# Optimization experiments

Measured on AMD Instinct MI355X. Metric: run time of the kernel, lower is better.

## Reference

```python
import jax, jax.numpy as jnp
import numpy as np

THRESHOLD = 0.95
B, T, H = 32, 2000, 512
NUM_TARGETS = 250.0  # alphas normalized so each row sums to this (mimics alpha *= num/_num)
MAX_LABEL_LEN = 256


def setup_inputs() -> dict:
    key = jax.random.key(0)
    k1, k2 = jax.random.split(key)
    hidden = jax.random.normal(k1, (B, T, H), dtype=jnp.float32)
    u = jax.random.uniform(k2, (B, T), dtype=jnp.float32)
    alphas = u / u.sum(-1, keepdims=True) * NUM_TARGETS  # per-row sum == NUM_TARGETS
    return {"hidden": hidden, "alphas": alphas, "max_label_len": MAX_LABEL_LEN}


def _cif(hidden, alphas, max_label_len, threshold=THRESHOLD):
    """Continuous integrate-and-fire: sequential scan over time + fire-gather."""
    Bn, Tn, Hn = hidden.shape

    def step(carry, inp):
        integrate, frame = carry              # [B], [B, H]
        alpha, h = inp                        # [B], [B, H]
        dist_completion = 1.0 - integrate
        integ = integrate + alpha
        fire = integ > threshold              # [B] bool
        cur = jnp.where(fire, dist_completion, alpha)
        remainds = alpha - cur
        frame_out = frame + cur[:, None] * h  # emitted frame at this step
        integ_next = jnp.where(fire, integ - 1.0, integ)
        frame_next = jnp.where(fire[:, None], remainds[:, None] * h, frame_out)
        return (integ_next, frame_next), (integ, frame_out)

    init = (jnp.zeros((Bn,), hidden.dtype), jnp.zeros((Bn, Hn), hidden.dtype))
    xs = (jnp.swapaxes(alphas, 0, 1), jnp.swapaxes(hidden, 0, 1))  # time-major
    _, (fires_t, frames_t) = jax.lax.scan(step, init, xs)
    fires = jnp.swapaxes(fires_t, 0, 1)    # [B, T]
    frames = jnp.swapaxes(frames_t, 0, 1)  # [B, T, H]

    # Gather fired frames per batch row, left-packed and zero-padded to max_label_len.
    mask = fires > threshold                               # [B, T]
    pos = jnp.cumsum(mask.astype(jnp.int32), axis=1) - 1   # running fire index
    pos = jnp.where(mask, pos, max_label_len)              # non-fires go to dump slot
    out = jnp.zeros((Bn, max_label_len + 1, Hn), hidden.dtype)
    out = out.at[jnp.arange(Bn)[:, None], pos].set(frames)
    return out[:, :max_label_len]  # drop dump slot -> [B, L, H]


def reference(hidden, alphas, max_label_len):
    return _cif(hidden, alphas, max_label_len)
```

## Files before the change

### kernel.cpp

```cpp
#include <hip/hip_runtime.h>
#include <stdint.h>

static constexpr int   Bn      = 32;
static constexpr int   Tn      = 2000;
static constexpr int   Hn      = 512;
static constexpr int   Ln      = 256;
static constexpr float kThresh = 0.95f;
static constexpr int   TCHUNK  = 40;
static constexpr int   NTCH    = Tn / TCHUNK;
static constexpr int   PCH     = 20;
static constexpr int   NPCH    = Tn / PCH;
static constexpr int   MSTRIDE = 64;
static constexpr unsigned PUBF = 0x40000000u;

__global__ __launch_bounds__(64, 1) void cif_fused_kernel(
    const float* __restrict__ hidden,
    const float* __restrict__ alphas,
    uint64_t* __restrict__ meta,
    float* __restrict__ out) {
  const int lane = threadIdx.x;
  __shared__ __align__(16) float alds[Tn];

  if (blockIdx.x < Bn) {
    __builtin_amdgcn_s_setprio(3);
    const int b = blockIdx.x;
    {
      const float4* __restrict__ arow =
          reinterpret_cast<const float4*>(alphas + (size_t)b * Tn);
      for (int i = lane; i < Tn / 4; i += 64)
        *reinterpret_cast<float4*>(&alds[4 * i]) = arow[i];
    }
    __syncthreads();

    float I  = 0.0f;
    int   fc = 0;
    float cur[PCH], nxt[PCH];
#pragma unroll
    for (int i = 0; i < PCH / 4; ++i) {
      const float4 v = *reinterpret_cast<const float4*>(&alds[4 * i]);
      cur[4 * i + 0] = v.x; cur[4 * i + 1] = v.y;
      cur[4 * i + 2] = v.z; cur[4 * i + 3] = v.w;
    }
    for (int c = 0; c < NPCH; ++c) {
      if (c + 1 < NPCH) {
#pragma unroll
        for (int i = 0; i < PCH / 4; ++i) {
          const float4 v = *reinterpret_cast<const float4*>(
              &alds[(c + 1) * PCH + 4 * i]);
          nxt[4 * i + 0] = v.x; nxt[4 * i + 1] = v.y;
          nxt[4 * i + 2] = v.z; nxt[4 * i + 3] = v.w;
        }
      }
      if ((c & 1) == 0 && lane == 0) {
        const uint64_t v = ((uint64_t)__float_as_uint(I) << 32) |
                           (uint64_t)(PUBF | (unsigned)fc);
        __hip_atomic_store(&meta[(size_t)b * MSTRIDE + (c >> 1)], v,
                           __ATOMIC_RELAXED, __HIP_MEMORY_SCOPE_AGENT);
      }
#pragma unroll
      for (int j = 0; j < PCH; ++j) {
        const float integ = I + cur[j];
        const bool  fire  = integ > kThresh;
        I  = fire ? (integ - 1.0f) : integ;
        fc += fire ? 1 : 0;
      }
#pragma unroll
      for (int i = 0; i < PCH; ++i) cur[i] = nxt[i];
    }
    return;
  }

  const int idx = blockIdx.x - Bn;
  const int b   = idx & (Bn - 1);
  const int tc  = idx >> 5;
  const int t_start = tc * TCHUNK;
  const int col = lane * 8;

  auto wait_meta = [&](int c) -> uint64_t {
    const uint64_t* p = &meta[(size_t)b * MSTRIDE + c];
    uint64_t v;
    for (;;) {
      v = __hip_atomic_load(p, __ATOMIC_RELAXED, __HIP_MEMORY_SCOPE_AGENT);
      if ((unsigned)v & PUBF) break;
      __builtin_amdgcn_s_sleep(16);
    }
    return v;
  };

  const float* __restrict__ arow = alphas + (size_t)b * Tn;

  float I; int s;
  if (tc == 0) { I = 0.0f; s = 0; }
  else {
    const uint64_t v = wait_meta(tc);
    I = __uint_as_float((unsigned)(v >> 32));
    s = (int)((unsigned)v & 0xFFFFu);
  }

  int   t_prev   = -1;
  float rem_prev = 0.0f;
  for (int k = 1; tc - k >= 0 && t_prev < 0; ++k) {
    const int ck = tc - k;
    float Ik;
    if (ck == 0) Ik = 0.0f;
    else {
      const uint64_t v = wait_meta(ck);
      Ik = __uint_as_float((unsigned)(v >> 32));
    }
    const float* __restrict__ ap = arow + ck * TCHUNK;
    int lt = -1; float lrem = 0.0f;
#pragma unroll
    for (int j = 0; j < TCHUNK; ++j) {
      const float a     = ap[j];
      const float integ = Ik + a;
      const bool  fire  = integ > kThresh;
      if (fire) { lt = ck * TCHUNK + j; lrem = a - (1.0f - Ik); }
      Ik = fire ? (integ - 1.0f) : integ;
    }
    if (lt >= 0) { t_prev = lt; rem_prev = lrem; }
  }

  const float* __restrict__ hb = hidden + (size_t)b * Tn * Hn + col;
  float4 acc0 = make_float4(0.f, 0.f, 0.f, 0.f);
  float4 acc1 = make_float4(0.f, 0.f, 0.f, 0.f);
  float4 h0, h1;

  auto loadh = [&](int t) {
    h0 = *reinterpret_cast<const float4*>(hb + (size_t)t * Hn);
    h1 = *reinterpret_cast<const float4*>(hb + (size_t)t * Hn + 4);
  };
  auto acc8 = [&](float wt) {
    acc0.x += wt * h0.x; acc0.y += wt * h0.y;
    acc0.z += wt * h0.z; acc0.w += wt * h0.w;
    acc1.x += wt * h1.x; acc1.y += wt * h1.y;
    acc1.z += wt * h1.z; acc1.w += wt * h1.w;
  };
  auto set8 = [&](float wt) {
    acc0.x = wt * h0.x; acc0.y = wt * h0.y;
    acc0.z = wt * h0.z; acc0.w = wt * h0.w;
    acc1.x = wt * h1.x; acc1.y = wt * h1.y;
    acc1.z = wt * h1.z; acc1.w = wt * h1.w;
  };

  if (t_prev >= 0) {
    loadh(t_prev);
    set8(rem_prev);
  }
  for (int t = t_prev + 1; t < t_start; ++t) {
    loadh(t);
    acc8(arow[t]);
  }

  for (int j = 0; j < TCHUNK; ++j) {
    const int   t     = t_start + j;
    const float a     = arow[t];
    const float integ = I + a;
    const bool  fire  = integ > kThresh;
    loadh(t);
    if (fire) {
      const float cw = 1.0f - I;
      acc8(cw);
      if (s < Ln) {
        float* op = out + ((size_t)b * Ln + s) * Hn + col;
        *reinterpret_cast<float4*>(op)     = acc0;
        *reinterpret_cast<float4*>(op + 4) = acc1;
      }
      const float rem = a - cw;
      set8(rem);
      s += 1;
      I  = integ - 1.0f;
    } else {
      acc8(a);
      I = integ;
    }
  }
  if (tc == NTCH - 1) {
    const float4 z = make_float4(0.f, 0.f, 0.f, 0.f);
    for (int s2 = s; s2 < Ln; ++s2) {
      float* op = out + ((size_t)b * Ln + s2) * Hn + col;
      *reinterpret_cast<float4*>(op)     = z;
      *reinterpret_cast<float4*>(op + 4) = z;
    }
  }
}

extern "C" void kernel_launch(void* const* d_in, const int* in_sizes, int n_in,
                              void* d_out, int out_size, void* d_ws, size_t ws_size,
                              hipStream_t stream) {
  const float* hidden = (const float*)d_in[0];
  const float* alphas = (const float*)d_in[1];
  float* out = (float*)d_out;

  uint64_t* meta = (uint64_t*)d_ws;
  hipMemsetAsync(meta, 0, (size_t)Bn * MSTRIDE * sizeof(uint64_t), stream);

  const int nblocks = Bn + NTCH * Bn;
  cif_fused_kernel<<<nblocks, 64, 0, stream>>>(hidden, alphas, meta, out);
}
```

Before: 63.80 us.

## Double chunk size and stream scan alphas through rolling float4 prefetch

Doubles the per-block time chunk from 40 to 80, which halves the number of worker blocks and metadata slots. The scan block now keeps four float4 registers in a rolling prefetch from LDS instead of a 20-element double buffer, and it publishes prefix state every 80 steps. The LDS array gets a zero pad so the prefetch can read past the end safely. The aim is to cut per-chunk overhead and register pressure on the serial scan. The cost is less parallelism and more serial work per block, and the backward search loop is no longer unrolled.

```diff
diff --git a/kernel.cpp b/kernel.cpp
--- a/kernel.cpp
+++ b/kernel.cpp
@@ -6,11 +6,9 @@
 static constexpr int   Hn      = 512;
 static constexpr int   Ln      = 256;
 static constexpr float kThresh = 0.95f;
-static constexpr int   TCHUNK  = 40;
+static constexpr int   TCHUNK  = 80;
 static constexpr int   NTCH    = Tn / TCHUNK;
-static constexpr int   PCH     = 20;
-static constexpr int   NPCH    = Tn / PCH;
-static constexpr int   MSTRIDE = 64;
+static constexpr int   MSTRIDE = 32;
 static constexpr unsigned PUBF = 0x40000000u;
 
 __global__ __launch_bounds__(64, 1) void cif_fused_kernel(
@@ -19,7 +17,7 @@
     uint64_t* __restrict__ meta,
     float* __restrict__ out) {
   const int lane = threadIdx.x;
-  __shared__ __align__(16) float alds[Tn];
+  __shared__ __align__(16) float alds[Tn + 64];
 
   if (blockIdx.x < Bn) {
     __builtin_amdgcn_s_setprio(3);
@@ -29,43 +27,43 @@
           reinterpret_cast<const float4*>(alphas + (size_t)b * Tn);
       for (int i = lane; i < Tn / 4; i += 64)
         *reinterpret_cast<float4*>(&alds[4 * i]) = arow[i];
+      for (int i = Tn / 4 + lane; i < (Tn + 64) / 4; i += 64)
+        *reinterpret_cast<float4*>(&alds[4 * i]) =
+            make_float4(0.f, 0.f, 0.f, 0.f);
     }
     __syncthreads();
 
+    const float4* __restrict__ lds4 =
+        reinterpret_cast<const float4*>(&alds[0]);
     float I  = 0.0f;
     int   fc = 0;
-    float cur[PCH], nxt[PCH];
+
+    float4 q0 = lds4[0], q1 = lds4[1], q2 = lds4[2], q3 = lds4[3];
+    int rd = 4;
+
+    auto step4 = [&](const float4& q) {
 #pragma unroll
-    for (int i = 0; i < PCH / 4; ++i) {
-      const float4 v = *reinterpret_cast<const float4*>(&alds[4 * i]);
-      cur[4 * i + 0] = v.x; cur[4 * i + 1] = v.y;
-      cur[4 * i + 2] = v.z; cur[4 * i + 3] = v.w;
-    }
-    for (int c = 0; c < NPCH; ++c) {
-      if (c + 1 < NPCH) {
-#pragma unroll
-        for (int i = 0; i < PCH / 4; ++i) {
-          const float4 v = *reinterpret_cast<const float4*>(
-              &alds[(c + 1) * PCH + 4 * i]);
-          nxt[4 * i + 0] = v.x; nxt[4 * i + 1] = v.y;
-          nxt[4 * i + 2] = v.z; nxt[4 * i + 3] = v.w;
-        }
-      }
-      if ((c & 1) == 0 && lane == 0) {
-        const uint64_t v = ((uint64_t)__float_as_uint(I) << 32) |
-                           (uint64_t)(PUBF | (unsigned)fc);
-        __hip_atomic_store(&meta[(size_t)b * MSTRIDE + (c >> 1)], v,
-                           __ATOMIC_RELAXED, __HIP_MEMORY_SCOPE_AGENT);
-      }
-#pragma unroll
-      for (int j = 0; j < PCH; ++j) {
-        const float integ = I + cur[j];
+      for (int j = 0; j < 4; ++j) {
+        const float a = (j == 0) ? q.x : (j == 1) ? q.y : (j == 2) ? q.z : q.w;
+        const float integ = I + a;
         const bool  fire  = integ > kThresh;
         I  = fire ? (integ - 1.0f) : integ;
         fc += fire ? 1 : 0;
       }
-#pragma unroll
-      for (int i = 0; i < PCH; ++i) cur[i] = nxt[i];
+    };
+
+    for (int c = 0; c < 125; ++c) {
+      if (lane == 0 && (c % 5) == 0) {
+        const uint64_t v = ((uint64_t)__float_as_uint(I) << 32) |
+                           (uint64_t)(PUBF | (unsigned)fc);
+        __hip_atomic_store(&meta[(size_t)b * MSTRIDE + c / 5], v,
+                           __ATOMIC_RELAXED, __HIP_MEMORY_SCOPE_AGENT);
+      }
+      step4(q0); q0 = lds4[rd + 0];
+      step4(q1); q1 = lds4[rd + 1];
+      step4(q2); q2 = lds4[rd + 2];
+      step4(q3); q3 = lds4[rd + 3];
+      rd += 4;
     }
     return;
   }
@@ -109,7 +107,6 @@
     }
     const float* __restrict__ ap = arow + ck * TCHUNK;
     int lt = -1; float lrem = 0.0f;
-#pragma unroll
     for (int j = 0; j < TCHUNK; ++j) {
       const float a     = ap[j];
       const float integ = Ik + a;
```

Result: slower. 78.14 us (+22.5%).
